# Kernel optimization log

Hardware: AMD Instinct MI355X
Metric: run time of the kernel (lower is better)

Reference implementation:

```python
import jax, jax.numpy as jnp
import numpy as np

B, S, NK, H, D, DM = 2, 2048, 32, 8, 64, 512
NEG = -1e9


def setup_inputs() -> dict:
    key = jax.random.key(0)
    ks = jax.random.split(key, 12)
    hidden_states = jax.random.normal(ks[0], (B, S, DM), jnp.float32)
    rpe = jax.random.normal(ks[1], (B, S, NK, H), jnp.float32)
    idx = jax.random.randint(ks[2], (S, NK), 0, S)
    pad = jax.random.uniform(ks[3], (S, NK)) < 0.1
    q_k_mask = jnp.where(pad, -1, idx).astype(jnp.int32)
    k_q_mask = jax.random.randint(ks[4], (S, NK), 0, S).astype(jnp.int32)  # only used by TVM backward
    sc = 0.02
    w_q = jax.random.normal(ks[5], (DM, H * D), jnp.float32) * sc
    w_k = jax.random.normal(ks[6], (DM, H * D), jnp.float32) * sc
    w_v = jax.random.normal(ks[7], (DM, H * D), jnp.float32) * sc
    fc_w = jax.random.normal(ks[8], (H * D, DM), jnp.float32) * sc
    fc_b = jnp.zeros((DM,), jnp.float32)
    ln_g = jnp.ones((DM,), jnp.float32)
    ln_b = jnp.zeros((DM,), jnp.float32)
    return {"hidden_states": hidden_states, "rpe": rpe, "q_k_mask": q_k_mask,
            "k_q_mask": k_q_mask, "w_q": w_q, "w_k": w_k, "w_v": w_v,
            "fc_w": fc_w, "fc_b": fc_b, "ln_g": ln_g, "ln_b": ln_b}


def reference(hidden_states, rpe, q_k_mask, k_q_mask, w_q, w_k, w_v, fc_w, fc_b, ln_g, ln_b):
    bsz, seq_len, _ = hidden_states.shape
    q = (hidden_states @ w_q).reshape(bsz, seq_len, H, D)
    k = (hidden_states @ w_k).reshape(bsz, seq_len, H, D)
    v = (hidden_states @ w_v).reshape(bsz, seq_len, H, D)

    valid = q_k_mask >= 0                      # [S, NK]
    idx = jnp.where(valid, q_k_mask, 0)        # safe gather index
    vmask = valid[None, :, None, :]            # [1,S,1,NK] broadcast over (b, h)

    # QKP_mm_tvm: sparse QK^T over neighbor lists, plus relative-position bias,
    # padded slots -> -1e9.  k_g: [B,S,NK,H,D]
    k_g = k[:, idx]
    scores = jnp.einsum('bshd,bsnhd->bshn', q, k_g) + rpe.transpose(0, 1, 3, 2)
    scores = jnp.where(vmask, scores, NEG)
    scores = scores / (D ** 0.5)

    attn = jax.nn.softmax(scores, axis=-1)
    # AttnV_mm_tvm with padding 0: padded slots contribute nothing.
    attn = attn * vmask
    v_g = v[:, idx]                            # [B,S,NK,H,D]
    ctx = jnp.einsum('bshn,bsnhd->bshd', attn, v_g).reshape(bsz, seq_len, H * D)

    out = ctx @ fc_w + fc_b + hidden_states    # dropout = identity (eval)
    mu = jnp.mean(out, axis=-1, keepdims=True)
    var = jnp.mean((out - mu) ** 2, axis=-1, keepdims=True)
    return (out - mu) * jax.lax.rsqrt(var + 1e-6) * ln_g + ln_b
```

## Files before the change

### kernel.cpp

```cpp
#include <hip/hip_runtime.h>
#include <hip/hip_bf16.h>

constexpr int Bb  = 2;
constexpr int Ss  = 2048;
constexpr int NKk = 32;
constexpr int Hh  = 8;
constexpr int DMm = 512;
constexpr int Mm  = Bb * Ss;
constexpr int QKV = 1536;

typedef __attribute__((ext_vector_type(8))) short bf16x8;
typedef __attribute__((ext_vector_type(4))) float f32x4;
typedef _Float16 f16x2 __attribute__((ext_vector_type(2)));

__device__ __forceinline__ float b2f(unsigned short u) {
  return __uint_as_float((unsigned)u << 16);
}
__device__ __forceinline__ unsigned short f2b(float f) {
  unsigned u = __float_as_uint(f);
  unsigned r = (u + 0x7fffu + ((u >> 16) & 1u)) >> 16;
  return (unsigned short)r;
}
__device__ __forceinline__ ushort f2h(float f) {
  _Float16 h = (_Float16)f;
  return __builtin_bit_cast(ushort, h);
}
__device__ __forceinline__ void gload_lds16(const ushort* g, ushort* l) {
  __builtin_amdgcn_global_load_lds(
      (const __attribute__((address_space(1))) void*)g,
      (__attribute__((address_space(3))) void*)l, 16, 0, 0);
}
__device__ __forceinline__ float dot2h(uint a2, uint b2, float c) {
#if __has_builtin(__builtin_amdgcn_fdot2)
  return __builtin_amdgcn_fdot2(__builtin_bit_cast(f16x2, a2),
                                __builtin_bit_cast(f16x2, b2), c, false);
#else
  const f16x2 a = __builtin_bit_cast(f16x2, a2);
  const f16x2 b = __builtin_bit_cast(f16x2, b2);
  return c + (float)a.x * (float)b.x + (float)a.y * (float)b.y;
#endif
}

__global__ __launch_bounds__(256) void cvt_all_k(
    const float* __restrict__ hs,
    const float* __restrict__ Wq, const float* __restrict__ Wk,
    const float* __restrict__ Wv, const float* __restrict__ Wf,
    ushort* __restrict__ Xb, ushort* __restrict__ Wt3, ushort* __restrict__ Wtf)
{
  __shared__ float tile[64][65];
  const int z = blockIdx.z;
  const int t = threadIdx.x;

  if (z >= 4) {
    const int cid = (z - 4) * 64 + blockIdx.x * 8 + blockIdx.y;
    const size_t base8 = (size_t)cid * 1024;
#pragma unroll
    for (int it = 0; it < 4; ++it) {
      const size_t i = base8 + it * 256 + t;
      const float4 a = reinterpret_cast<const float4*>(hs)[2 * i];
      const float4 b = reinterpret_cast<const float4*>(hs)[2 * i + 1];
      ushort o[8] = {f2b(a.x), f2b(a.y), f2b(a.z), f2b(a.w),
                     f2b(b.x), f2b(b.y), f2b(b.z), f2b(b.w)};
      reinterpret_cast<uint4*>(Xb)[i] = *reinterpret_cast<uint4*>(o);
    }
    return;
  }

  const float* W = (z == 0) ? Wq : (z == 1) ? Wk : (z == 2) ? Wv : Wf;
  ushort* Wt = (z < 3) ? (Wt3 + (size_t)z * 512 * 512) : Wtf;

  const int k0 = blockIdx.x * 64, n0 = blockIdx.y * 64;
#pragma unroll
  for (int p = 0; p < 4; ++p) {
    const int r = (t >> 4) + p * 16, c = (t & 15) * 4;
    const float4 v = *reinterpret_cast<const float4*>(&W[(size_t)(k0 + r) * 512 + n0 + c]);
    tile[r][c] = v.x; tile[r][c + 1] = v.y; tile[r][c + 2] = v.z; tile[r][c + 3] = v.w;
  }
  __syncthreads();
  const int n = t >> 2, ks = (t & 3) * 16;
  ushort o[16];
#pragma unroll
  for (int i = 0; i < 16; ++i) o[i] = f2b(tile[ks + i][n]);
  *reinterpret_cast<uint4*>(&Wt[(size_t)(n0 + n) * 512 + k0 + ks])     = *reinterpret_cast<uint4*>(&o[0]);
  *reinterpret_cast<uint4*>(&Wt[(size_t)(n0 + n) * 512 + k0 + ks + 8]) = *reinterpret_cast<uint4*>(&o[8]);
}

template <int OUTM, int BMv, int BNv>
__global__ __launch_bounds__(256) void gemm_pipe(
    const ushort* __restrict__ Xb, const ushort* __restrict__ Wt,
    void* __restrict__ Yv, const float* __restrict__ bias,
    const float* __restrict__ resid, int ldY)
{
  constexpr int MI  = BMv / 32;
  constexpr int NJ  = BNv / 32;
  constexpr int STG = MI + NJ;
  constexpr int ASZ = BMv * 64;
  __shared__ ushort smem[2 * ASZ + 2 * BNv * 64];

  const int bm = blockIdx.x * BMv;
  const int bn = blockIdx.y * BNv;
  const int t  = threadIdx.x;
  const int wave = t >> 6, lane = t & 63;
  const int wm = (wave >> 1) * (BMv / 2);
  const int wn = (wave & 1) * (BNv / 2);

  f32x4 acc[MI][NJ] = {};

  auto stage = [&](int buf, int k0) {
    ushort* A = smem + buf * ASZ;
    ushort* B = smem + 2 * ASZ + buf * (BNv * 64);
#pragma unroll
    for (int p = 0; p < MI; ++p) {
      const int i = p * 256 + t;
      const int row = i >> 3, sb = i & 7;
      gload_lds16(Xb + (size_t)(bm + row) * 512 + k0 + ((sb ^ (row & 7)) << 3),
                  &A[(size_t)(p * 256 + wave * 64) * 8]);
    }
#pragma unroll
    for (int p = 0; p < NJ; ++p) {
      const int i = p * 256 + t;
      const int row = i >> 3, sb = i & 7;
      gload_lds16(Wt + (size_t)(bn + row) * 512 + k0 + ((sb ^ (row & 7)) << 3),
                  &B[(size_t)(p * 256 + wave * 64) * 8]);
    }
  };

  auto compute = [&](int buf) {
    const ushort* A = smem + buf * ASZ;
    const ushort* B = smem + 2 * ASZ + buf * (BNv * 64);
#pragma unroll
    for (int ks = 0; ks < 2; ++ks) {
      const int kb = ks * 4 + (lane >> 4);
      bf16x8 af[MI], bfr[NJ];
#pragma unroll
      for (int i = 0; i < MI; ++i) {
        const int row = wm + i * 16 + (lane & 15);
        af[i] = *reinterpret_cast<const bf16x8*>(&A[row * 64 + ((kb ^ (row & 7)) << 3)]);
      }
#pragma unroll
      for (int j = 0; j < NJ; ++j) {
        const int row = wn + j * 16 + (lane & 15);
        bfr[j] = *reinterpret_cast<const bf16x8*>(&B[row * 64 + ((kb ^ (row & 7)) << 3)]);
      }
#pragma unroll
      for (int i = 0; i < MI; ++i)
#pragma unroll
        for (int j = 0; j < NJ; ++j)
          acc[i][j] = __builtin_amdgcn_mfma_f32_16x16x32_bf16(af[i], bfr[j], acc[i][j], 0, 0, 0);
    }
  };

  stage(0, 0);
  int cur = 0;
#pragma unroll
  for (int i = 0; i < 8; ++i) {
    if (i < 7) {
      stage(cur ^ 1, (i + 1) * 64);
      asm volatile("s_waitcnt vmcnt(%0)" :: "n"(STG) : "memory");
    } else {
      asm volatile("s_waitcnt vmcnt(0)" ::: "memory");
    }
    __builtin_amdgcn_sched_barrier(0);
    __builtin_amdgcn_s_barrier();
    compute(cur);
    __builtin_amdgcn_sched_barrier(0);
    __builtin_amdgcn_s_barrier();
    cur ^= 1;
  }

  if (OUTM) {
#pragma unroll
    for (int i = 0; i < MI; ++i)
#pragma unroll
      for (int j = 0; j < NJ; ++j)
#pragma unroll
        for (int r = 0; r < 4; ++r) {
          const int row = wm + i * 16 + (lane >> 4) * 4 + r;
          const int col = wn + j * 16 + (lane & 15);
          smem[row * BNv + col] = f2h(acc[i][j][r]);
        }
    __syncthreads();
    ushort* Y = reinterpret_cast<ushort*>(Yv);
    constexpr int CPT = BMv * BNv / 8 / 256;
#pragma unroll
    for (int p = 0; p < CPT; ++p) {
      const int c = p * 256 + t;
      const int row = c / (BNv / 8);
      const int cb  = c % (BNv / 8);
      *reinterpret_cast<uint4*>(&Y[(size_t)(bm + row) * ldY + bn + cb * 8]) =
          *reinterpret_cast<uint4*>(&smem[row * BNv + cb * 8]);
    }
  } else {
    float* Y = reinterpret_cast<float*>(Yv);
#pragma unroll
    for (int i = 0; i < MI; ++i) {
#pragma unroll
      for (int j = 0; j < NJ; ++j) {
        const int m = bm + wm + i * 16 + (lane >> 4) * 4;
        const int n = bn + wn + j * 16 + (lane & 15);
        const float bb = bias[n];
#pragma unroll
        for (int r = 0; r < 4; ++r)
          Y[(size_t)(m + r) * ldY + n] = acc[i][j][r] + bb + resid[(size_t)(m + r) * 512 + n];
      }
    }
  }
}

__global__ __launch_bounds__(256) void attn_f16(
    const ushort* __restrict__ qkv, const float* __restrict__ rpe,
    const int* __restrict__ qkm, ushort* __restrict__ ctx)
{
  __shared__ ushort Ks[32 * 512];
  __shared__ uint   qs[256];

  const int bs = blockIdx.x;
  const int b  = bs >> 11;
  const int s  = bs & 2047;
  const int t  = threadIdx.x;
  const int wv = t >> 6, lane = t & 63;

  qs[t] = *reinterpret_cast<const uint*>(qkv + (size_t)bs * QKV + 2 * t);

#pragma unroll
  for (int r = 0; r < 8; ++r) {
    const int n = r * 4 + wv;
    int im = qkm[s * NKk + n];
    im = im < 0 ? 0 : im;
    const ushort* gsrc = qkv + (size_t)(b * Ss + im) * QKV + 512
                       + ((lane ^ (n & 7)) * 8);
    gload_lds16(gsrc, &Ks[n * 512]);
  }

  const int iv = qkm[s * NKk + (lane & 31)];
  const float rv = rpe[((size_t)bs * NKk + (t & 31)) * Hh + (t >> 5)];

  __syncthreads();

  const ushort* vbase = qkv + (size_t)b * Ss * QKV + 1024;
  const int e = 2 * t;
  uint vvu[32];
#pragma unroll
  for (int n2 = 0; n2 < 32; ++n2) {
    int row = __shfl(iv, (lane & 32) + n2, 64);
    row = row < 0 ? 0 : row;
    vvu[n2] = *reinterpret_cast<const uint*>(&vbase[(size_t)row * QKV + (e & 511)]);
  }

  const int h = t >> 5;
  const int n = t & 31;
  const bool valid = (iv >= 0);

  float acc0 = 0.f, acc1 = 0.f;
#pragma unroll
  for (int j = 0; j < 8; ++j) {
    const int blk = (h * 8 + j) ^ (n & 7);
    const uint4 kk = *reinterpret_cast<const uint4*>(&Ks[n * 512 + blk * 8]);
    const uint4 qq = *reinterpret_cast<const uint4*>(&qs[h * 32 + j * 4]);
    acc0 = dot2h(qq.x, kk.x, acc0);
    acc1 = dot2h(qq.y, kk.y, acc1);
    acc0 = dot2h(qq.z, kk.z, acc0);
    acc1 = dot2h(qq.w, kk.w, acc1);
  }
  float sc = acc0 + acc1 + rv;
  sc = valid ? sc * 0.125f : -1e30f;

  float mx = sc;
#pragma unroll
  for (int m = 16; m >= 1; m >>= 1) mx = fmaxf(mx, __shfl_xor(mx, m, 32));
  const float p = valid ? __expf(sc - mx) : 0.f;
  float sum = p;
#pragma unroll
  for (int m = 16; m >= 1; m >>= 1) sum += __shfl_xor(sum, m, 32);
  const float pn = (sum > 0.f) ? (p / sum) : 0.f;

  f16x2 a2;
  a2.x = (_Float16)pn;
  a2.y = a2.x;
  const int av = __builtin_bit_cast(int, a2);
  f16x2 c01 = {(_Float16)0.f, (_Float16)0.f};
#pragma unroll
  for (int n2 = 0; n2 < 32; ++n2) {
    const int aw = __shfl(av, (lane & 32) + n2, 64);
    c01 += __builtin_bit_cast(f16x2, aw) * __builtin_bit_cast(f16x2, vvu[n2]);
  }
  const uint packed = (uint)f2b((float)c01.x) | ((uint)f2b((float)c01.y) << 16);
  *reinterpret_cast<uint*>(&ctx[(size_t)bs * 512 + e]) = packed;
}

__global__ __launch_bounds__(256) void ln_k(
    float* __restrict__ x, const float* __restrict__ g,
    const float* __restrict__ bta)
{
  const int w    = threadIdx.x >> 6;
  const int lane = threadIdx.x & 63;
  const int row  = blockIdx.x * 4 + w;

  float4* xr = reinterpret_cast<float4*>(x + (size_t)row * 512);
  const float4 v0 = xr[lane];
  const float4 v1 = xr[lane + 64];

  float sum = v0.x + v0.y + v0.z + v0.w + v1.x + v1.y + v1.z + v1.w;
  float sq  = v0.x * v0.x + v0.y * v0.y + v0.z * v0.z + v0.w * v0.w
            + v1.x * v1.x + v1.y * v1.y + v1.z * v1.z + v1.w * v1.w;
#pragma unroll
  for (int m = 32; m >= 1; m >>= 1) {
    sum += __shfl_xor(sum, m, 64);
    sq  += __shfl_xor(sq,  m, 64);
  }
  const float mu  = sum * (1.f / 512.f);
  const float var = sq * (1.f / 512.f) - mu * mu;
  const float rs  = rsqrtf(var + 1e-6f);

  const float4 g0 = reinterpret_cast<const float4*>(g)[lane];
  const float4 g1 = reinterpret_cast<const float4*>(g)[lane + 64];
  const float4 b0 = reinterpret_cast<const float4*>(bta)[lane];
  const float4 b1 = reinterpret_cast<const float4*>(bta)[lane + 64];

  float4 o0, o1;
  o0.x = (v0.x - mu) * rs * g0.x + b0.x;
  o0.y = (v0.y - mu) * rs * g0.y + b0.y;
  o0.z = (v0.z - mu) * rs * g0.z + b0.z;
  o0.w = (v0.w - mu) * rs * g0.w + b0.w;
  o1.x = (v1.x - mu) * rs * g1.x + b1.x;
  o1.y = (v1.y - mu) * rs * g1.y + b1.y;
  o1.z = (v1.z - mu) * rs * g1.z + b1.z;
  o1.w = (v1.w - mu) * rs * g1.w + b1.w;
  xr[lane]      = o0;
  xr[lane + 64] = o1;
}

extern "C" void kernel_launch(void* const* d_in, const int* in_sizes, int n_in,
                              void* d_out, int out_size, void* d_ws, size_t ws_size,
                              hipStream_t stream) {
  const float* hs  = (const float*)d_in[0];
  const float* rpe = (const float*)d_in[1];
  const int*   qkm = (const int*)d_in[2];
  const float* wq  = (const float*)d_in[4];
  const float* wk  = (const float*)d_in[5];
  const float* wv  = (const float*)d_in[6];
  const float* fcw = (const float*)d_in[7];
  const float* fcb = (const float*)d_in[8];
  const float* lng = (const float*)d_in[9];
  const float* lnb = (const float*)d_in[10];
  float* out = (float*)d_out;

  ushort* Xb  = (ushort*)d_ws;
  ushort* Wt3 = Xb  + (size_t)Mm * DMm;
  ushort* Wtf = Wt3 + (size_t)3 * DMm * DMm;
  ushort* qkv = Wtf + (size_t)DMm * DMm;
  ushort* cxb = qkv + (size_t)Mm * QKV;

  cvt_all_k<<<dim3(8, 8, 8), 256, 0, stream>>>(hs, wq, wk, wv, fcw, Xb, Wt3, Wtf);

  gemm_pipe<1, 128, 96><<<dim3(Mm / 128, QKV / 96), 256, 0, stream>>>(
      Xb, Wt3, qkv, nullptr, nullptr, QKV);

  attn_f16<<<Mm, 256, 0, stream>>>(qkv, rpe, qkm, cxb);

  gemm_pipe<0, 128, 64><<<dim3(Mm / 128, DMm / 64), 256, 0, stream>>>(
      cxb, Wtf, out, fcb, hs, DMm);
  ln_k<<<Mm / 4, 256, 0, stream>>>(out, lng, lnb);
}
```

Before: 54.95 us.

## Fuse hidden-state bf16 conversion into QKV GEMM with triple-buffered fp32 staging

The QKV GEMM now loads the fp32 hidden states straight into LDS and converts them to bf16 with packed convert instructions while building MFMA fragments. This removes the separate conversion pass and the bf16 copy of X held in the workspace. The K tile drops to 32 and the pipeline moves to three buffers with deeper prefetch. In exchange the A tiles move twice the bytes per element from global memory, and each tile does redundant conversion work across blocks that share the same rows.

```diff
diff --git a/kernel.cpp b/kernel.cpp
--- a/kernel.cpp
+++ b/kernel.cpp
@@ -25,7 +25,12 @@
   _Float16 h = (_Float16)f;
   return __builtin_bit_cast(ushort, h);
 }
-__device__ __forceinline__ void gload_lds16(const ushort* g, ushort* l) {
+__device__ __forceinline__ uint cvtpk_bf16(float lo, float hi) {
+  uint r;
+  asm("v_cvt_pk_bf16_f32 %0, %1, %2" : "=v"(r) : "v"(lo), "v"(hi));
+  return r;
+}
+__device__ __forceinline__ void gload_lds16(const void* g, void* l) {
   __builtin_amdgcn_global_load_lds(
       (const __attribute__((address_space(1))) void*)g,
       (__attribute__((address_space(3))) void*)l, 16, 0, 0);
@@ -41,31 +46,14 @@
 #endif
 }
 
-__global__ __launch_bounds__(256) void cvt_all_k(
-    const float* __restrict__ hs,
+__global__ __launch_bounds__(256) void cvt_w_k(
     const float* __restrict__ Wq, const float* __restrict__ Wk,
     const float* __restrict__ Wv, const float* __restrict__ Wf,
-    ushort* __restrict__ Xb, ushort* __restrict__ Wt3, ushort* __restrict__ Wtf)
+    ushort* __restrict__ Wt3, ushort* __restrict__ Wtf)
 {
   __shared__ float tile[64][65];
   const int z = blockIdx.z;
   const int t = threadIdx.x;
-
-  if (z >= 4) {
-    const int cid = (z - 4) * 64 + blockIdx.x * 8 + blockIdx.y;
-    const size_t base8 = (size_t)cid * 1024;
-#pragma unroll
-    for (int it = 0; it < 4; ++it) {
-      const size_t i = base8 + it * 256 + t;
-      const float4 a = reinterpret_cast<const float4*>(hs)[2 * i];
-      const float4 b = reinterpret_cast<const float4*>(hs)[2 * i + 1];
-      ushort o[8] = {f2b(a.x), f2b(a.y), f2b(a.z), f2b(a.w),
-                     f2b(b.x), f2b(b.y), f2b(b.z), f2b(b.w)};
-      reinterpret_cast<uint4*>(Xb)[i] = *reinterpret_cast<uint4*>(o);
-    }
-    return;
-  }
-
   const float* W = (z == 0) ? Wq : (z == 1) ? Wk : (z == 2) ? Wv : Wf;
   ushort* Wt = (z < 3) ? (Wt3 + (size_t)z * 512 * 512) : Wtf;
 
@@ -85,30 +73,125 @@
   *reinterpret_cast<uint4*>(&Wt[(size_t)(n0 + n) * 512 + k0 + ks + 8]) = *reinterpret_cast<uint4*>(&o[8]);
 }
 
-template <int OUTM, int BMv, int BNv>
-__global__ __launch_bounds__(256) void gemm_pipe(
-    const ushort* __restrict__ Xb, const ushort* __restrict__ Wt,
-    void* __restrict__ Yv, const float* __restrict__ bias,
-    const float* __restrict__ resid, int ldY)
+__global__ __launch_bounds__(256) void gemm_qkv(
+    const float* __restrict__ hs, const ushort* __restrict__ Wt,
+    ushort* __restrict__ Y)
 {
-  constexpr int MI  = BMv / 32;
-  constexpr int NJ  = BNv / 32;
-  constexpr int STG = MI + NJ;
-  constexpr int ASZ = BMv * 64;
-  __shared__ ushort smem[2 * ASZ + 2 * BNv * 64];
-
-  const int bm = blockIdx.x * BMv;
-  const int bn = blockIdx.y * BNv;
+  __shared__ float  Asm[3][128 * 32];
+  __shared__ ushort Bsm[3][128 * 32];
+
+  const int bm = blockIdx.x * 128;
+  const int bn = blockIdx.y * 96;
   const int t  = threadIdx.x;
   const int wave = t >> 6, lane = t & 63;
-  const int wm = (wave >> 1) * (BMv / 2);
-  const int wn = (wave & 1) * (BNv / 2);
+  const int wm = (wave >> 1) * 64;
+  const int wn = (wave & 1) * 48;
+
+  f32x4 acc[4][3] = {};
+
+  auto stage = [&](int buf, int k0) {
+#pragma unroll
+    for (int p = 0; p < 4; ++p) {
+      const int i = p * 256 + t;
+      const int row = i >> 3, sb = i & 7;
+      gload_lds16(hs + (size_t)(bm + row) * 512 + k0 + ((sb ^ (row & 7)) << 2),
+                  &Asm[buf][(size_t)(p * 256 + wave * 64) * 4]);
+    }
+#pragma unroll
+    for (int p = 0; p < 2; ++p) {
+      const int i = p * 256 + t;
+      const int row = i >> 2, sb = i & 3;
+      gload_lds16(Wt + (size_t)(bn + row) * 512 + k0 + ((sb ^ (row & 3)) << 3),
+                  &Bsm[buf][(size_t)(p * 256 + wave * 64) * 8]);
+    }
+  };
+
+  auto compute = [&](int buf) {
+    const int kb = lane >> 4, r16 = lane & 15;
+    bf16x8 af[4], bfr[3];
+#pragma unroll
+    for (int i = 0; i < 4; ++i) {
+      const int row = wm + i * 16 + r16;
+      const int b0 = (2 * kb) ^ (row & 7), b1 = (2 * kb + 1) ^ (row & 7);
+      const float4 fa = *reinterpret_cast<const float4*>(&Asm[buf][row * 32 + b0 * 4]);
+      const float4 fb = *reinterpret_cast<const float4*>(&Asm[buf][row * 32 + b1 * 4]);
+      uint u[4] = {cvtpk_bf16(fa.x, fa.y), cvtpk_bf16(fa.z, fa.w),
+                   cvtpk_bf16(fb.x, fb.y), cvtpk_bf16(fb.z, fb.w)};
+      af[i] = __builtin_bit_cast(bf16x8, *reinterpret_cast<uint4*>(u));
+    }
+#pragma unroll
+    for (int j = 0; j < 3; ++j) {
+      const int row = wn + j * 16 + r16;
+      const int bb = kb ^ (row & 3);
+      bfr[j] = *reinterpret_cast<const bf16x8*>(&Bsm[buf][row * 32 + bb * 8]);
+    }
+#pragma unroll
+    for (int i = 0; i < 4; ++i)
+#pragma unroll
+      for (int j = 0; j < 3; ++j)
+        acc[i][j] = __builtin_amdgcn_mfma_f32_16x16x32_bf16(af[i], bfr[j], acc[i][j], 0, 0, 0);
+  };
+
+  stage(0, 0);
+  stage(1, 32);
+#pragma unroll
+  for (int i = 0; i < 16; ++i) {
+    if (i < 14) {
+      stage((i + 2) % 3, (i + 2) * 32);
+      asm volatile("s_waitcnt vmcnt(12)" ::: "memory");
+    } else if (i == 14) {
+      asm volatile("s_waitcnt vmcnt(6)" ::: "memory");
+    } else {
+      asm volatile("s_waitcnt vmcnt(0)" ::: "memory");
+    }
+    __builtin_amdgcn_sched_barrier(0);
+    __builtin_amdgcn_s_barrier();
+    compute(i % 3);
+    __builtin_amdgcn_sched_barrier(0);
+    __builtin_amdgcn_s_barrier();
+  }
+
+  ushort* rep = reinterpret_cast<ushort*>(&Asm[0][0]);
+#pragma unroll
+  for (int i = 0; i < 4; ++i)
+#pragma unroll
+    for (int j = 0; j < 3; ++j)
+#pragma unroll
+      for (int r = 0; r < 4; ++r) {
+        const int row = wm + i * 16 + (lane >> 4) * 4 + r;
+        const int col = wn + j * 16 + (lane & 15);
+        rep[row * 96 + col] = f2h(acc[i][j][r]);
+      }
+  __syncthreads();
+#pragma unroll
+  for (int p = 0; p < 6; ++p) {
+    const int c = p * 256 + t;
+    const int row = c / 12, cb = c % 12;
+    *reinterpret_cast<uint4*>(&Y[(size_t)(bm + row) * QKV + bn + cb * 8]) =
+        *reinterpret_cast<uint4*>(&rep[row * 96 + cb * 8]);
+  }
+}
+
+__global__ __launch_bounds__(256) void gemm_fc(
+    const ushort* __restrict__ Xb, const ushort* __restrict__ Wt,
+    float* __restrict__ Y, const float* __restrict__ bias,
+    const float* __restrict__ resid)
+{
+  constexpr int MI = 4, NJ = 2, STG = 6, ASZ = 128 * 64;
+  __shared__ ushort smem[2 * ASZ + 2 * 64 * 64];
+
+  const int bm = blockIdx.x * 128;
+  const int bn = blockIdx.y * 64;
+  const int t  = threadIdx.x;
+  const int wave = t >> 6, lane = t & 63;
+  const int wm = (wave >> 1) * 64;
+  const int wn = (wave & 1) * 32;
 
   f32x4 acc[MI][NJ] = {};
 
   auto stage = [&](int buf, int k0) {
     ushort* A = smem + buf * ASZ;
-    ushort* B = smem + 2 * ASZ + buf * (BNv * 64);
+    ushort* B = smem + 2 * ASZ + buf * (64 * 64);
 #pragma unroll
     for (int p = 0; p < MI; ++p) {
       const int i = p * 256 + t;
@@ -127,7 +210,7 @@
 
   auto compute = [&](int buf) {
     const ushort* A = smem + buf * ASZ;
-    const ushort* B = smem + 2 * ASZ + buf * (BNv * 64);
+    const ushort* B = smem + 2 * ASZ + buf * (64 * 64);
 #pragma unroll
     for (int ks = 0; ks < 2; ++ks) {
       const int kb = ks * 4 + (lane >> 4);
@@ -168,41 +251,16 @@
     cur ^= 1;
   }
 
-  if (OUTM) {
-#pragma unroll
-    for (int i = 0; i < MI; ++i)
-#pragma unroll
-      for (int j = 0; j < NJ; ++j)
-#pragma unroll
-        for (int r = 0; r < 4; ++r) {
-          const int row = wm + i * 16 + (lane >> 4) * 4 + r;
-          const int col = wn + j * 16 + (lane & 15);
-          smem[row * BNv + col] = f2h(acc[i][j][r]);
-        }
-    __syncthreads();
-    ushort* Y = reinterpret_cast<ushort*>(Yv);
-    constexpr int CPT = BMv * BNv / 8 / 256;
-#pragma unroll
-    for (int p = 0; p < CPT; ++p) {
-      const int c = p * 256 + t;
-      const int row = c / (BNv / 8);
-      const int cb  = c % (BNv / 8);
-      *reinterpret_cast<uint4*>(&Y[(size_t)(bm + row) * ldY + bn + cb * 8]) =
-          *reinterpret_cast<uint4*>(&smem[row * BNv + cb * 8]);
-    }
-  } else {
-    float* Y = reinterpret_cast<float*>(Yv);
-#pragma unroll
-    for (int i = 0; i < MI; ++i) {
-#pragma unroll
-      for (int j = 0; j < NJ; ++j) {
-        const int m = bm + wm + i * 16 + (lane >> 4) * 4;
-        const int n = bn + wn + j * 16 + (lane & 15);
-        const float bb = bias[n];
-#pragma unroll
-        for (int r = 0; r < 4; ++r)
-          Y[(size_t)(m + r) * ldY + n] = acc[i][j][r] + bb + resid[(size_t)(m + r) * 512 + n];
-      }
+#pragma unroll
+  for (int i = 0; i < MI; ++i) {
+#pragma unroll
+    for (int j = 0; j < NJ; ++j) {
+      const int m = bm + wm + i * 16 + (lane >> 4) * 4;
+      const int n = bn + wn + j * 16 + (lane & 15);
+      const float bb = bias[n];
+#pragma unroll
+      for (int r = 0; r < 4; ++r)
+        Y[(size_t)(m + r) * 512 + n] = acc[i][j][r] + bb + resid[(size_t)(m + r) * 512 + n];
     }
   }
 }
@@ -345,20 +403,17 @@
   const float* lnb = (const float*)d_in[10];
   float* out = (float*)d_out;
 
-  ushort* Xb  = (ushort*)d_ws;
-  ushort* Wt3 = Xb  + (size_t)Mm * DMm;
+  ushort* Wt3 = (ushort*)d_ws;
   ushort* Wtf = Wt3 + (size_t)3 * DMm * DMm;
   ushort* qkv = Wtf + (size_t)DMm * DMm;
   ushort* cxb = qkv + (size_t)Mm * QKV;
 
-  cvt_all_k<<<dim3(8, 8, 8), 256, 0, stream>>>(hs, wq, wk, wv, fcw, Xb, Wt3, Wtf);
-
-  gemm_pipe<1, 128, 96><<<dim3(Mm / 128, QKV / 96), 256, 0, stream>>>(
-      Xb, Wt3, qkv, nullptr, nullptr, QKV);
+  cvt_w_k<<<dim3(8, 8, 4), 256, 0, stream>>>(wq, wk, wv, fcw, Wt3, Wtf);
+
+  gemm_qkv<<<dim3(Mm / 128, QKV / 96), 256, 0, stream>>>(hs, Wt3, qkv);
 
   attn_f16<<<Mm, 256, 0, stream>>>(qkv, rpe, qkm, cxb);
 
-  gemm_pipe<0, 128, 64><<<dim3(Mm / 128, DMm / 64), 256, 0, stream>>>(
-      cxb, Wtf, out, fcb, hs, DMm);
+  gemm_fc<<<dim3(Mm / 128, DMm / 64), 256, 0, stream>>>(cxb, Wtf, out, fcb, hs);
   ln_k<<<Mm / 4, 256, 0, stream>>>(out, lng, lnb);
 }
```

New measurement: 60.00 us. +9.2%, slower.
